# Performance work log

Measured on AMD Instinct MI355X. Metric: run time of the kernel, lower is better.

## Reference

```python
import jax, jax.numpy as jnp
import numpy as np

# ---- grid / camera configuration (from init_kwargs) ----
OGH, OGW = 896, 1600          # camera image size
DOWNSAMPLE = 16
FH, FW = OGH // DOWNSAMPLE, OGW // DOWNSAMPLE  # 56, 100
DMIN, DMAX, DSTEP = 1.0, 60.0, 0.125           # dbound
XB = (1.0, 41.0, 0.25)
YB = (-20.0, 20.0, 0.25)
ZB = (-10.0, 10.0, 20.0)
NX = int((XB[1] - XB[0]) / XB[2])  # 160
NY = int((YB[1] - YB[0]) / YB[2])  # 160
DX = jnp.array([XB[2], YB[2], ZB[2]], dtype=jnp.float32)
BX = jnp.array([XB[0] + XB[2] / 2.0, YB[0] + YB[2] / 2.0, ZB[0] + ZB[2] / 2.0], dtype=jnp.float32)
LO = BX - DX / 2.0  # grid lower corner per axis
BOUNDS_LO = jnp.array([XB[0], YB[0], ZB[0]], dtype=jnp.float32)
BOUNDS_HI = jnp.array([XB[1], YB[1], ZB[1]], dtype=jnp.float32)
NVOX = jnp.array([NX, NY, 1], dtype=jnp.int32)


def setup_inputs() -> dict:
    key = jax.random.key(0)
    k1, k2, k3 = jax.random.split(key, 3)
    B, D, C = 8, 472, 472
    depth_logits = jax.random.normal(k1, (B, D, FH, FW), dtype=jnp.float32)
    features = jax.random.normal(k2, (B, C, FH, FW), dtype=jnp.float32)
    # realistic pinhole intrinsics (invertible)
    fx, fy = 800.0, 800.0
    cx, cy = OGW / 2.0, OGH / 2.0
    K = jnp.array([[fx, 0.0, cx], [0.0, fy, cy], [0.0, 0.0, 1.0]], dtype=jnp.float32)
    intrins = jnp.tile(K[None], (B, 1, 1))
    # small per-batch yaw rotations (camera->ego)
    ang = jnp.linspace(-0.1, 0.1, B)
    ca, sa = jnp.cos(ang), jnp.sin(ang)
    z = jnp.zeros_like(ca)
    o = jnp.ones_like(ca)
    rotMtx = jnp.stack([
        jnp.stack([ca, -sa, z], -1),
        jnp.stack([sa, ca, z], -1),
        jnp.stack([z, z, o], -1),
    ], axis=1).astype(jnp.float32)
    return {"depth_logits": depth_logits, "features": features,
            "intrins": intrins, "rotMtx": rotMtx}


def _forward(depth_logits, features, intrins, rotMtx):
    B, D, Hd, Wd = depth_logits.shape
    C = features.shape[1]
    # depth distribution (softmax over depth bins), then argmax depth (abs_depth=False)
    depth = jax.nn.softmax(depth_logits, axis=1)
    dmax_idx = jnp.argmax(depth, axis=1)                      # [B,Hd,Wd]
    d = dmax_idx.astype(depth_logits.dtype) * DSTEP + DMIN    # metric depth per pixel
    # frustum uv grid (torch.linspace endpoints 0..ogf inclusive)
    xs = jnp.linspace(0.0, OGW, Wd, dtype=jnp.float32)
    ys = jnp.linspace(0.0, OGH, Hd, dtype=jnp.float32)
    u = jnp.broadcast_to(xs[None, None, :], (B, Hd, Wd))
    v = jnp.broadcast_to(ys[None, :, None], (B, Hd, Wd))
    uvd = jnp.stack([u * d, v * d, d], axis=-1)               # [B,Hd,Wd,3]
    # [x,y,z] = R K^{-1} [u*d, v*d, d]
    combine = jnp.matmul(rotMtx, jnp.linalg.inv(intrins))     # [B,3,3]
    pc = jnp.einsum('bij,bhwj->bhwi', combine, uvd)           # [B,Hd,Wd,3]
    # voxel pooling (scatter features into BEV grid)
    N = Hd * Wd
    pcf = pc.reshape(B, N, 3)
    feats = features.transpose(0, 2, 3, 1).reshape(B, N, C)
    in_bounds = jnp.all((pcf > BOUNDS_LO) & (pcf < BOUNDS_HI), axis=-1)
    vox = jnp.floor((pcf - LO) / DX).astype(jnp.int32)        # [B,N,3]
    in_grid = jnp.all((vox >= 0) & (vox < NVOX), axis=-1)
    valid = in_bounds & in_grid                               # [B,N]
    b_off = jnp.arange(B, dtype=jnp.int32)[:, None] * (NX * NY)
    flat = b_off + vox[..., 0] * NY + vox[..., 1]             # [B,N]
    flat = jnp.where(valid, flat, 0).reshape(-1)
    w = valid.astype(feats.dtype)[..., None]
    bev = jax.ops.segment_sum((feats * w).reshape(-1, C), flat,
                              num_segments=B * NX * NY)
    return bev.reshape(B, NX, NY, C)


def reference(depth_logits, features, intrins, rotMtx):
    return _forward(depth_logits, features, intrins, rotMtx)
```

## Files before the change

kernel.cpp:

```cpp
#include <hip/hip_runtime.h>
#include <math.h>

#define BB 8
#define DD 472
#define CC 472
#define FH 56
#define FW 100
#define NPIX (FH * FW)
#define NPIX_TOT (BB * NPIX)
#define NX 160
#define NY 160

__global__ void k_combine(const float* __restrict__ intrins,
                          const float* __restrict__ rot,
                          double* __restrict__ combine) {
    int b = threadIdx.x;
    if (b >= BB) return;
    const float* K = intrins + b * 9;
    const float* R = rot + b * 9;
    double a00 = K[0], a01 = K[1], a02 = K[2];
    double a10 = K[3], a11 = K[4], a12 = K[5];
    double a20 = K[6], a21 = K[7], a22 = K[8];
    double det = a00 * (a11 * a22 - a12 * a21)
               - a01 * (a10 * a22 - a12 * a20)
               + a02 * (a10 * a21 - a11 * a20);
    double inv[9];
    inv[0] =  (a11 * a22 - a12 * a21) / det;
    inv[1] = -(a01 * a22 - a02 * a21) / det;
    inv[2] =  (a01 * a12 - a02 * a11) / det;
    inv[3] = -(a10 * a22 - a12 * a20) / det;
    inv[4] =  (a00 * a22 - a02 * a20) / det;
    inv[5] = -(a00 * a12 - a02 * a10) / det;
    inv[6] =  (a10 * a21 - a11 * a20) / det;
    inv[7] = -(a00 * a21 - a01 * a20) / det;
    inv[8] =  (a00 * a11 - a01 * a10) / det;
    for (int i = 0; i < 3; ++i)
        for (int j = 0; j < 3; ++j) {
            double s = 0.0;
            for (int k = 0; k < 3; ++k) s += (double)R[i * 3 + k] * inv[k * 3 + j];
            combine[b * 9 + i * 3 + j] = s;
        }
}

__global__ __launch_bounds__(256) void k_cells(const float* __restrict__ dlog,
                                               const double* __restrict__ combine,
                                               int* __restrict__ cells) {
    __shared__ float s_best[4][64];
    __shared__ int   s_idx[4][64];
    const int lane = threadIdx.x & 63;
    const int q = threadIdx.x >> 6;
    const int pid = blockIdx.x * 64 + lane;
    const int b = pid / NPIX;
    const int rem = pid - b * NPIX;

    const float* base = dlog + (size_t)b * DD * NPIX + rem;
    float best = -INFINITY;
    int bi = 0;
    const int d0 = q * 118;
    #pragma unroll 4
    for (int k = 0; k < 118; ++k) {
        int dd = d0 + k;
        float v = base[(size_t)dd * NPIX];
        if (v > best) { best = v; bi = dd; }
    }
    s_best[q][lane] = best;
    s_idx[q][lane] = bi;
    __syncthreads();
    if (q != 0) return;

    for (int qq = 1; qq < 4; ++qq) {
        float v = s_best[qq][lane];
        if (v > best) { best = v; bi = s_idx[qq][lane]; }
    }

    const int h = rem / FW;
    const int w = rem - h * FW;
    double d = (double)bi * 0.125 + 1.0;
    double u = (double)w * (1600.0 / 99.0);
    double v2 = (double)h * (896.0 / 55.0);
    double x0 = u * d, x1 = v2 * d, x2 = d;
    const double* M = combine + b * 9;
    double px = M[0] * x0 + M[1] * x1 + M[2] * x2;
    double py = M[3] * x0 + M[4] * x1 + M[5] * x2;
    double pz = M[6] * x0 + M[7] * x1 + M[8] * x2;

    bool ok = (px > 1.0) && (px < 41.0) &&
              (py > -20.0) && (py < 20.0) &&
              (pz > -10.0) && (pz < 10.0);
    int vx = (int)floor((px - 1.0) / 0.25);
    int vy = (int)floor((py + 20.0) / 0.25);
    int vz = (int)floor((pz + 10.0) / 20.0);
    ok = ok && (vx >= 0) && (vx < NX) && (vy >= 0) && (vy < NY) &&
         (vz >= 0) && (vz < 1);
    cells[pid] = ok ? (b * (NX * NY) + vx * NY + vy) : -1;
}

__global__ __launch_bounds__(256) void k_scatter(const float* __restrict__ feats,
                                                 const int* __restrict__ cells,
                                                 float* __restrict__ out) {
    const int tile = blockIdx.x;
    const int wi = threadIdx.x & 15;
    const int ci0 = threadIdx.x >> 4;
    const int pid = tile * 16 + wi;
    const int cell = cells[pid];

    if (!__any(cell >= 0)) return;
    if (cell < 0) return;

    const int b = pid / NPIX;
    const int rem = pid - b * NPIX;
    const float* fb = feats + (size_t)b * CC * NPIX + rem;
    float* ob = out + (size_t)cell * CC;
    for (int c = ci0; c < CC; c += 16) {
        atomicAdd(ob + c, fb[(size_t)c * NPIX]);
    }
}

extern "C" void kernel_launch(void* const* d_in, const int* in_sizes, int n_in,
                              void* d_out, int out_size, void* d_ws, size_t ws_size,
                              hipStream_t stream) {
    const float* dlog    = (const float*)d_in[0];
    const float* feats   = (const float*)d_in[1];
    const float* intrins = (const float*)d_in[2];
    const float* rot     = (const float*)d_in[3];
    float* out = (float*)d_out;

    int* cells = (int*)d_ws;
    double* combine = (double*)((char*)d_ws + (((size_t)NPIX_TOT * 4 + 255) & ~(size_t)255));

    hipMemsetAsync(d_out, 0, (size_t)out_size * sizeof(float), stream);

    k_combine<<<1, 64, 0, stream>>>(intrins, rot, combine);
    k_cells<<<NPIX_TOT / 64, 256, 0, stream>>>(dlog, combine, cells);
    k_scatter<<<NPIX_TOT / 16, 256, 0, stream>>>(feats, cells, out);
}
```

Baseline: 508.6 us.

## Fuse output zeroing, matrix inverse and depth argmax into one kernel

Merges the memset of the BEV output, the per-batch camera matrix computation and the depth argmax/voxel-cell kernel into a single launch. Extra blocks zero the output with float4 stores while the other blocks run the argmax, and each argmax block recomputes the 3x3 inverse into shared memory. The aim is to cut launch overhead and overlap the roughly 387 MB zero-fill with the depth-logit reads. In exchange, every cell block repeats the small double-precision inverse, and the zeroing blocks compete with the argmax blocks for memory bandwidth.

```diff
diff --git a/kernel.cpp b/kernel.cpp
--- a/kernel.cpp
+++ b/kernel.cpp
@@ -10,43 +10,58 @@
 #define NPIX_TOT (BB * NPIX)
 #define NX 160
 #define NY 160
+#define OUT_FLOATS ((size_t)BB * NX * NY * CC)
+#define OUT_F4 (OUT_FLOATS / 4)
+#define CELL_BLOCKS (NPIX_TOT / 64)
+#define ZERO_BLOCKS 2048
 
-__global__ void k_combine(const float* __restrict__ intrins,
-                          const float* __restrict__ rot,
-                          double* __restrict__ combine) {
-    int b = threadIdx.x;
-    if (b >= BB) return;
-    const float* K = intrins + b * 9;
-    const float* R = rot + b * 9;
-    double a00 = K[0], a01 = K[1], a02 = K[2];
-    double a10 = K[3], a11 = K[4], a12 = K[5];
-    double a20 = K[6], a21 = K[7], a22 = K[8];
-    double det = a00 * (a11 * a22 - a12 * a21)
-               - a01 * (a10 * a22 - a12 * a20)
-               + a02 * (a10 * a21 - a11 * a20);
-    double inv[9];
-    inv[0] =  (a11 * a22 - a12 * a21) / det;
-    inv[1] = -(a01 * a22 - a02 * a21) / det;
-    inv[2] =  (a01 * a12 - a02 * a11) / det;
-    inv[3] = -(a10 * a22 - a12 * a20) / det;
-    inv[4] =  (a00 * a22 - a02 * a20) / det;
-    inv[5] = -(a00 * a12 - a02 * a10) / det;
-    inv[6] =  (a10 * a21 - a11 * a20) / det;
-    inv[7] = -(a00 * a21 - a01 * a20) / det;
-    inv[8] =  (a00 * a11 - a01 * a10) / det;
-    for (int i = 0; i < 3; ++i)
-        for (int j = 0; j < 3; ++j) {
-            double s = 0.0;
-            for (int k = 0; k < 3; ++k) s += (double)R[i * 3 + k] * inv[k * 3 + j];
-            combine[b * 9 + i * 3 + j] = s;
-        }
-}
+__global__ __launch_bounds__(256) void k_main(const float* __restrict__ dlog,
+                                              const float* __restrict__ intrins,
+                                              const float* __restrict__ rot,
+                                              float* __restrict__ out,
+                                              int* __restrict__ cells) {
+    if (blockIdx.x >= CELL_BLOCKS) {
+        size_t tid = (size_t)(blockIdx.x - CELL_BLOCKS) * 256 + threadIdx.x;
+        float4* o4 = (float4*)out;
+        const float4 z = make_float4(0.f, 0.f, 0.f, 0.f);
+        const size_t stride = (size_t)ZERO_BLOCKS * 256;
+        for (size_t i = tid; i < OUT_F4; i += stride) o4[i] = z;
+        return;
+    }
 
-__global__ __launch_bounds__(256) void k_cells(const float* __restrict__ dlog,
-                                               const double* __restrict__ combine,
-                                               int* __restrict__ cells) {
+    __shared__ double sM[BB][9];
     __shared__ float s_best[4][64];
     __shared__ int   s_idx[4][64];
+
+    if (threadIdx.x < BB) {
+        const int b = threadIdx.x;
+        const float* K = intrins + b * 9;
+        const float* R = rot + b * 9;
+        double a00 = K[0], a01 = K[1], a02 = K[2];
+        double a10 = K[3], a11 = K[4], a12 = K[5];
+        double a20 = K[6], a21 = K[7], a22 = K[8];
+        double det = a00 * (a11 * a22 - a12 * a21)
+                   - a01 * (a10 * a22 - a12 * a20)
+                   + a02 * (a10 * a21 - a11 * a20);
+        double inv[9];
+        inv[0] =  (a11 * a22 - a12 * a21) / det;
+        inv[1] = -(a01 * a22 - a02 * a21) / det;
+        inv[2] =  (a01 * a12 - a02 * a11) / det;
+        inv[3] = -(a10 * a22 - a12 * a20) / det;
+        inv[4] =  (a00 * a22 - a02 * a20) / det;
+        inv[5] = -(a00 * a12 - a02 * a10) / det;
+        inv[6] =  (a10 * a21 - a11 * a20) / det;
+        inv[7] = -(a00 * a21 - a01 * a20) / det;
+        inv[8] =  (a00 * a11 - a01 * a10) / det;
+        for (int i = 0; i < 3; ++i)
+            for (int j = 0; j < 3; ++j) {
+                double s = 0.0;
+                for (int k = 0; k < 3; ++k)
+                    s += (double)R[i * 3 + k] * inv[k * 3 + j];
+                sM[b][i * 3 + j] = s;
+            }
+    }
+
     const int lane = threadIdx.x & 63;
     const int q = threadIdx.x >> 6;
     const int pid = blockIdx.x * 64 + lane;
@@ -79,7 +94,7 @@
     double u = (double)w * (1600.0 / 99.0);
     double v2 = (double)h * (896.0 / 55.0);
     double x0 = u * d, x1 = v2 * d, x2 = d;
-    const double* M = combine + b * 9;
+    const double* M = sM[b];
     double px = M[0] * x0 + M[1] * x1 + M[2] * x2;
     double py = M[3] * x0 + M[4] * x1 + M[5] * x2;
     double pz = M[6] * x0 + M[7] * x1 + M[8] * x2;
@@ -124,13 +139,8 @@
     const float* intrins = (const float*)d_in[2];
     const float* rot     = (const float*)d_in[3];
     float* out = (float*)d_out;
+    int* cells = (int*)d_ws;
 
-    int* cells = (int*)d_ws;
-    double* combine = (double*)((char*)d_ws + (((size_t)NPIX_TOT * 4 + 255) & ~(size_t)255));
-
-    hipMemsetAsync(d_out, 0, (size_t)out_size * sizeof(float), stream);
-
-    k_combine<<<1, 64, 0, stream>>>(intrins, rot, combine);
-    k_cells<<<NPIX_TOT / 64, 256, 0, stream>>>(dlog, combine, cells);
+    k_main<<<CELL_BLOCKS + ZERO_BLOCKS, 256, 0, stream>>>(dlog, intrins, rot, out, cells);
     k_scatter<<<NPIX_TOT / 16, 256, 0, stream>>>(feats, cells, out);
 }
```

After: 517.0 us. No clear change (+1.6%).
